# Kernel optimization log

Measured on AMD Instinct MI355X. Metric: run time of the kernel, lower is better.

The kernel has to match this reference:

```python
import jax, jax.numpy as jnp
import numpy as np

EMBED_DIM = 1536
NUM_HEADS = 12
HEAD_DIM = EMBED_DIM // NUM_HEADS  # 128
SEQ = 2048
EPS = 1e-5


def rms_norm(x, w):
    # x: (..., HEAD_DIM)
    var = jnp.mean(jnp.square(x), axis=-1, keepdims=True)
    return x * jax.lax.rsqrt(var + EPS) * w


def apply_rotary(x, cos, sin):
    # x: (b, s, h, d); cos/sin: (s, d/2) -> broadcast (1, s, 1, d/2)
    d2 = cos.shape[-1]
    c = cos[None, :, None, :]
    s_ = sin[None, :, None, :]
    x1, x2 = x[..., :d2], x[..., d2:]
    return jnp.concatenate([x1 * c - x2 * s_, x2 * c + x1 * s_], axis=-1)


def setup_inputs() -> dict:
    key = jax.random.key(0)
    ks = jax.random.split(key, 10)
    x = jax.random.normal(ks[0], (SEQ, 1, EMBED_DIM), dtype=jnp.float32)
    cu_seqlens = jnp.array([0, SEQ // 2, SEQ], dtype=jnp.int32)
    # rotary tables for positions 0..SEQ-1, rotary dim = HEAD_DIM
    inv_freq = 1.0 / (10000.0 ** (jnp.arange(0, HEAD_DIM, 2, dtype=jnp.float32) / HEAD_DIM))
    pos = jnp.arange(SEQ, dtype=jnp.float32)
    freqs = pos[:, None] * inv_freq[None, :]  # (s, d/2)
    rotary_pos_emb_cos = jnp.cos(freqs)
    rotary_pos_emb_sin = jnp.sin(freqs)
    scale = 0.02
    w_qkv = jax.random.normal(ks[1], (EMBED_DIM, 3 * EMBED_DIM), dtype=jnp.float32) * scale
    b_qkv = jnp.zeros((3 * EMBED_DIM,), dtype=jnp.float32)
    q_norm_w = jnp.ones((HEAD_DIM,), dtype=jnp.float32)
    k_norm_w = jnp.ones((HEAD_DIM,), dtype=jnp.float32)
    w_proj = jax.random.normal(ks[2], (EMBED_DIM, EMBED_DIM), dtype=jnp.float32) * scale
    b_proj = jnp.zeros((EMBED_DIM,), dtype=jnp.float32)
    return {
        'x': x, 'cu_seqlens': cu_seqlens,
        'rotary_pos_emb_cos': rotary_pos_emb_cos, 'rotary_pos_emb_sin': rotary_pos_emb_sin,
        'w_qkv': w_qkv, 'b_qkv': b_qkv, 'q_norm_w': q_norm_w, 'k_norm_w': k_norm_w,
        'w_proj': w_proj, 'b_proj': b_proj,
    }


def reference(x, cu_seqlens, rotary_pos_emb_cos, rotary_pos_emb_sin,
              w_qkv, b_qkv, q_norm_w, k_norm_w, w_proj, b_proj):
    s, b, e = x.shape
    h, d = NUM_HEADS, HEAD_DIM
    qkv = jnp.einsum('sbe,ef->sbf', x, w_qkv) + b_qkv  # (s, b, 3e)
    q, k, v = jnp.split(qkv, 3, axis=2)
    q = q.reshape(s, b, h, d)
    k = k.reshape(s, b, h, d)
    v = v.reshape(s, b, h, d)
    # per-head RMSNorm on q/k
    q = rms_norm(q, q_norm_w)
    k = rms_norm(k, k_norm_w)
    # (s, b, h, d) -> (b, s, h, d)
    q = jnp.transpose(q, (1, 0, 2, 3))
    k = jnp.transpose(k, (1, 0, 2, 3))
    v = jnp.transpose(v, (1, 0, 2, 3))
    q = apply_rotary(q, rotary_pos_emb_cos, rotary_pos_emb_sin)
    k = apply_rotary(k, rotary_pos_emb_cos, rotary_pos_emb_sin)
    # varlen (block-diagonal, non-causal) attention via segment mask
    pos = jnp.arange(s)
    seg = jnp.searchsorted(cu_seqlens[1:], pos, side='right')  # (s,)
    mask = seg[:, None] == seg[None, :]  # (s, s)
    scale = d ** -0.5
    scores = jnp.einsum('bqhd,bkhd->bhqk', q, k) * scale  # (b, h, s, s)
    scores = jnp.where(mask[None, None, :, :], scores, jnp.finfo(scores.dtype).min)
    attn = jax.nn.softmax(scores, axis=-1)
    ctx = jnp.einsum('bhqk,bkhd->bqhd', attn, v)  # (b, s, h, d)
    # (b, s, h, d) -> (s, b, h*d)
    ctx = jnp.transpose(ctx, (1, 0, 2, 3)).reshape(s, b, h * d)
    out = jnp.einsum('sbe,ef->sbf', ctx, w_proj) + b_proj
    return out
```

## Files before the change

### kernel.cpp

```cpp
#include <hip/hip_runtime.h>
#include <hip/hip_bf16.h>
#include <stdint.h>

#define S_LEN 2048
#define EMB   1536
#define NH    12
#define HD    128
#define N3    4608
#define RMS_EPS 1e-5f
#define ATTN_SCALE 0.08838834764831845f
#define SPLIT 2
#define LOG2E 1.44269504088896f
#define DEFER_THR 11.5416f

typedef short short8_t __attribute__((ext_vector_type(8)));
typedef float f32x4    __attribute__((ext_vector_type(4)));

typedef __attribute__((address_space(1))) const void g1_void;
typedef __attribute__((address_space(3))) void l3_void;

__device__ __forceinline__ void gload_lds16(const void* g, void* l) {
  __builtin_amdgcn_global_load_lds((g1_void*)g, (l3_void*)l, 16, 0, 0);
}

__device__ __forceinline__ short f2bf(float f) {
  union { float f; unsigned u; } v; v.f = f;
  unsigned r = (v.u + 0x7FFFu + ((v.u >> 16) & 1u)) >> 16;
  return (short)(r & 0xFFFFu);
}
__device__ __forceinline__ float bf2f(short s) {
  union { unsigned u; float f; } v; v.u = ((unsigned)(unsigned short)s) << 16;
  return v.f;
}

__global__ __launch_bounds__(256) void k_cvt_bf16(const float* __restrict__ in,
                                                  short* __restrict__ out, int n) {
  int i = (blockIdx.x * 256 + threadIdx.x) * 4;
  if (i + 3 < n) {
    float4 v = *(const float4*)(in + i);
    short4 o;
    o.x = f2bf(v.x); o.y = f2bf(v.y); o.z = f2bf(v.z); o.w = f2bf(v.w);
    *(short4*)(out + i) = o;
  }
}

__global__ __launch_bounds__(256) void k_transpose_cvt(const float* __restrict__ W,
                                                       short* __restrict__ Wt,
                                                       int K, int N) {
  __shared__ float t[32][33];
  int n0 = blockIdx.x * 32, k0 = blockIdx.y * 32;
  int tx = threadIdx.x, ty = threadIdx.y;
#pragma unroll
  for (int r = 0; r < 4; ++r) {
    int k = ty + r * 8;
    t[k][tx] = W[(size_t)(k0 + k) * N + n0 + tx];
  }
  __syncthreads();
#pragma unroll
  for (int r = 0; r < 4; ++r) {
    int j = ty + r * 8;
    Wt[(size_t)(n0 + j) * K + k0 + tx] = f2bf(t[tx][j]);
  }
}

template<bool OBF>
__global__ __launch_bounds__(256, 2) void k_gemm_v7(const short* __restrict__ A,
                                                    const short* __restrict__ Bt,
                                                    const float* __restrict__ bias,
                                                    void* __restrict__ Cv,
                                                    int M, int N, int K) {
  __shared__ short lds[2][2][128 * 64];
  const int tid = threadIdx.x;
  const int lane = tid & 63, wid = tid >> 6;
  const int wr = (wid >> 1) * 64, wc = (wid & 1) * 64;

  const int nbn = N >> 7;
  const int perbn = nbn >> 2;
  const int x = blockIdx.x & 7;
  const int s = blockIdx.x >> 3;
  const int bm = ((x >> 2) * 8 + (s & 7)) * 128;
  const int bn = ((x & 3) * perbn + (s >> 3)) * 128;

  const int lr = lane & 15, lg = lane >> 4;
  const int swz = (lr & 7) << 4;
  const int srow = lane >> 3;
  const int skc  = ((lane & 7) ^ srow) * 8;

  f32x4 acc[4][4] = {};
  const int nk = K >> 6;

#define GSTAGE(kt_, buf_)                                                          \
  {                                                                                \
    const int kt__ = (kt_);                                                        \
    _Pragma("unroll")                                                              \
    for (int it = 0; it < 4; ++it) {                                               \
      int seg = wid * 4 + it;                                                      \
      int row = seg * 8 + srow;                                                    \
      gload_lds16(A  + (size_t)(bm + row) * K + kt__ + skc, &lds[buf_][0][seg * 512]); \
      gload_lds16(Bt + (size_t)(bn + row) * K + kt__ + skc, &lds[buf_][1][seg * 512]); \
    }                                                                              \
  }

  GSTAGE(0, 0);
  if (nk > 1) {
    GSTAGE(64, 1);
    asm volatile("s_waitcnt vmcnt(8)" ::: "memory");
  } else {
    asm volatile("s_waitcnt vmcnt(0)" ::: "memory");
  }
  __builtin_amdgcn_s_barrier();

  int cur = 0;
  for (int t = 0; t < nk; ++t) {
    const char* baseA = (const char*)&lds[cur][0][0];
    const char* baseB = (const char*)&lds[cur][1][0];

    short8_t af0[4], bf0[4], af1[4], bf1[4];
#pragma unroll
    for (int m = 0; m < 4; ++m) {
      int rowA = wr + m * 16 + lr;
      int rowB = wc + m * 16 + lr;
      af0[m] = *(const short8_t*)(baseA + ((rowA * 128 + 0 * 64 + lg * 16) ^ swz));
      bf0[m] = *(const short8_t*)(baseB + ((rowB * 128 + 0 * 64 + lg * 16) ^ swz));
      af1[m] = *(const short8_t*)(baseA + ((rowA * 128 + 1 * 64 + lg * 16) ^ swz));
      bf1[m] = *(const short8_t*)(baseB + ((rowB * 128 + 1 * 64 + lg * 16) ^ swz));
    }

    __builtin_amdgcn_s_setprio(1);
#pragma unroll
    for (int m = 0; m < 4; ++m)
#pragma unroll
      for (int n = 0; n < 4; ++n)
        acc[m][n] = __builtin_amdgcn_mfma_f32_16x16x32_bf16(af0[m], bf0[n], acc[m][n], 0, 0, 0);
    __builtin_amdgcn_s_setprio(0);

    asm volatile("s_waitcnt lgkmcnt(0)" ::: "memory");
    __builtin_amdgcn_sched_barrier(0);
    __builtin_amdgcn_s_barrier();

    if (t + 2 < nk) GSTAGE((t + 2) << 6, cur);

    __builtin_amdgcn_s_setprio(1);
#pragma unroll
    for (int m = 0; m < 4; ++m)
#pragma unroll
      for (int n = 0; n < 4; ++n)
        acc[m][n] = __builtin_amdgcn_mfma_f32_16x16x32_bf16(af1[m], bf1[n], acc[m][n], 0, 0, 0);
    __builtin_amdgcn_s_setprio(0);

    if (t + 2 < nk) {
      asm volatile("s_waitcnt vmcnt(8)" ::: "memory");
    } else {
      asm volatile("s_waitcnt vmcnt(0)" ::: "memory");
    }
    __builtin_amdgcn_s_barrier();
    cur ^= 1;
  }
#undef GSTAGE

#pragma unroll
  for (int m = 0; m < 4; ++m)
#pragma unroll
    for (int n = 0; n < 4; ++n) {
      int col = bn + wc + n * 16 + lr;
      float bv = bias[col];
#pragma unroll
      for (int r = 0; r < 4; ++r) {
        int row = bm + wr + m * 16 + lg * 4 + r;
        float v = acc[m][n][r] + bv;
        if (OBF) ((short*)Cv)[(size_t)row * N + col] = f2bf(v);
        else     ((float*)Cv)[(size_t)row * N + col] = v;
      }
    }
}

__global__ __launch_bounds__(256) void k_post(const short* __restrict__ qkv,
                                              const float* __restrict__ cosv,
                                              const float* __restrict__ sinv,
                                              const float* __restrict__ qw,
                                              const float* __restrict__ kw,
                                              short* __restrict__ qb,
                                              short* __restrict__ kb,
                                              short* __restrict__ vt) {
  __shared__ short ldsv[64 * 130];
  const int h = blockIdx.x, s0 = blockIdx.y * 64;
  const int t = threadIdx.x;
  const int r = t >> 2, j = t & 3;
  const int s = s0 + r;
  const size_t rowbase = (size_t)s * N3 + h * HD;
  const float SC2 = ATTN_SCALE * LOG2E;

  {
    const short* vp = qkv + rowbase + 2 * EMB + j * 32;
#pragma unroll
    for (int i4 = 0; i4 < 4; ++i4)
      *(short8_t*)&ldsv[r * 130 + j * 32 + i4 * 8] = *(const short8_t*)(vp + i4 * 8);
  }

#pragma unroll
  for (int qk = 0; qk < 2; ++qk) {
    const short* p = qkv + rowbase + qk * EMB + j * 32;
    const float* w = qk ? kw : qw;
    float v[32];
#pragma unroll
    for (int i4 = 0; i4 < 4; ++i4) {
      short8_t x = *(const short8_t*)(p + i4 * 8);
#pragma unroll
      for (int e = 0; e < 8; ++e) v[i4 * 8 + e] = bf2f(x[e]);
    }
    float ss = 0.f;
#pragma unroll
    for (int i = 0; i < 32; ++i) ss += v[i] * v[i];
    ss += __shfl_xor(ss, 1);
    ss += __shfl_xor(ss, 2);
    float rsq = rsqrtf(ss * (1.0f / HD) + RMS_EPS);
    if (qk == 0) rsq *= SC2;
#pragma unroll
    for (int i = 0; i < 32; ++i) v[i] = v[i] * rsq * w[j * 32 + i];
    const float* cp = cosv + (size_t)s * 64 + (j & 1) * 32;
    const float* sp = sinv + (size_t)s * 64 + (j & 1) * 32;
    short out[32];
#pragma unroll
    for (int i = 0; i < 32; ++i) {
      float part = __shfl_xor(v[i], 2);
      float c = cp[i], sn = sp[i];
      float o = (j < 2) ? (v[i] * c - part * sn) : (v[i] * c + part * sn);
      out[i] = f2bf(o);
    }
    short* dst = (qk ? kb : qb) + ((size_t)h * S_LEN + s) * HD + j * 32;
#pragma unroll
    for (int i4 = 0; i4 < 4; ++i4) {
      short8_t o8;
#pragma unroll
      for (int e = 0; e < 8; ++e) o8[e] = out[i4 * 8 + e];
      *(short8_t*)(dst + i4 * 8) = o8;
    }
  }

  __syncthreads();
  const int sl = t & 63, wv = t >> 6;
#pragma unroll
  for (int it = 0; it < 32; ++it) {
    int d = it * 4 + wv;
    vt[((size_t)h * HD + d) * S_LEN + s0 + sl] = ldsv[sl * 130 + d];
  }
}

__global__ __launch_bounds__(512, 2) void k_attn(const short* __restrict__ qb,
                                                 const short* __restrict__ kb,
                                                 const short* __restrict__ vt,
                                                 const int* __restrict__ cu, int nseg,
                                                 short* __restrict__ Opart,
                                                 float* __restrict__ mlpart) {
  __shared__ short ldsK[2][8192];
  __shared__ short ldsV[2][128 * 64];
  __shared__ short ldsP[8 * 16 * 64];

  const int wg = blockIdx.x;
  const int member = wg / 48;
  const int c = wg % 48;
  const int p = c & 1;
  const int h = c >> 2;
  const int qt = ((c >> 1) & 1) * 8 + member;

  const int q0 = qt * 128;
  const int tid = threadIdx.x, l = tid & 63, w = tid >> 6;
  const int lr = l & 15, lg = l >> 4;

  const short* kb_h = kb + (size_t)h * S_LEN * HD;
  const short* vt_h = vt + (size_t)h * HD * S_LEN;

  const int qrow_sm = q0 + w * 16 + lr;
  int segq = 0;
  for (int i = 1; i <= nseg; ++i) if (qrow_sm >= cu[i]) segq = i;
  const int rs_s = (segq == 0) ? 0 : cu[segq];
  const int re_s = (segq < nseg) ? cu[segq + 1] : S_LEN;
  float m = -INFINITY, lsum = 0.f;

  int seg0 = 0, seg1 = 0;
  for (int i = 1; i <= nseg; ++i) {
    if (q0 >= cu[i]) seg0 = i;
    if (q0 + 127 >= cu[i]) seg1 = i;
  }
  const int ks = (seg0 == 0) ? 0 : cu[seg0];
  const int ke = (seg1 < nseg) ? cu[seg1 + 1] : S_LEN;
  const int kt0 = (ks >> 6) << 6;
  const int nt = (ke - kt0 + 63) >> 6;
  const int tpb = (nt + SPLIT - 1) / SPLIT;
  const int tb0 = p * tpb;
  const int tb1 = (tb0 + tpb < nt) ? tb0 + tpb : nt;

  const int vseg_row = l >> 3;

  short8_t qf[4];
  {
    int srow = q0 + w * 16 + lr;
    const short* qp = qb + ((size_t)h * S_LEN + srow) * HD;
#pragma unroll
    for (int kk = 0; kk < 4; ++kk)
      qf[kk] = *(const short8_t*)(qp + kk * 32 + lg * 8);
  }

  f32x4 cacc[8] = {};

#define STAGE(kt_, buf_)                                                          \
  {                                                                               \
    const int kt__ = (kt_);                                                       \
    _Pragma("unroll")                                                             \
    for (int it = 0; it < 2; ++it) {                                              \
      int s = w * 2 + it;                                                         \
      int half = s >> 3;                                                          \
      int krow = (s & 7) * 8 + (l >> 3);                                          \
      int kc = half * 64 + (((l & 7) ^ (l >> 3)) * 8);                            \
      gload_lds16(kb_h + (size_t)(kt__ + krow) * HD + kc, &ldsK[buf_][s * 512]);  \
      int drow = s * 8 + vseg_row;                                                \
      int sv = ((l & 7) ^ (drow & 7)) * 8;                                        \
      gload_lds16(vt_h + (size_t)drow * S_LEN + kt__ + sv, &ldsV[buf_][s * 512]); \
    }                                                                             \
  }

  if (tb0 < tb1)     STAGE(kt0 + tb0 * 64, 0);
  if (tb0 + 1 < tb1) {
    STAGE(kt0 + (tb0 + 1) * 64, 1);
    asm volatile("s_waitcnt vmcnt(4)" ::: "memory");
  } else {
    asm volatile("s_waitcnt vmcnt(0)" ::: "memory");
  }
  __builtin_amdgcn_s_barrier();

  int cur = 0;
  for (int ti = tb0; ti < tb1; ++ti) {
    const int kt = kt0 + ti * 64;
    const char* bK = (const char*)&ldsK[cur][0];
    const char* bV = (const char*)&ldsV[cur][0];

    f32x4 sacc[4] = {};
    __builtin_amdgcn_s_setprio(1);
#pragma unroll
    for (int n = 0; n < 4; ++n) {
#pragma unroll
      for (int kk = 0; kk < 4; ++kk) {
        int row = n * 16 + lr;
        int byte = (kk >> 1) * 8192 + row * 128 + (kk & 1) * 64 + lg * 16;
        byte ^= (lr & 7) << 4;
        short8_t kf = *(const short8_t*)(bK + byte);
        sacc[n] = __builtin_amdgcn_mfma_f32_16x16x32_bf16(kf, qf[kk], sacc[n], 0, 0, 0);
      }
    }
    __builtin_amdgcn_s_setprio(0);

    if (!__all((kt >= rs_s) && (kt + 64 <= re_s))) {
#pragma unroll
      for (int n = 0; n < 4; ++n) {
        int kbase = kt + n * 16 + lg * 4;
#pragma unroll
        for (int r = 0; r < 4; ++r) {
          int key = kbase + r;
          sacc[n][r] = (key >= rs_s && key < re_s) ? sacc[n][r] : -1e30f;
        }
      }
    }

    float tm = sacc[0][0];
#pragma unroll
    for (int n = 0; n < 4; ++n)
#pragma unroll
      for (int r = 0; r < 4; ++r) tm = fmaxf(tm, sacc[n][r]);
    tm = fmaxf(tm, __shfl_xor(tm, 16));
    tm = fmaxf(tm, __shfl_xor(tm, 32));

    if (!__all(tm <= m + DEFER_THR)) {
      float mn = fmaxf(m, tm);
      float alpha = exp2f(m - mn);
      m = mn;
      lsum *= alpha;
      float a[4];
#pragma unroll
      for (int r = 0; r < 4; ++r) a[r] = __shfl(alpha, lg * 4 + r);
#pragma unroll
      for (int n = 0; n < 8; ++n)
#pragma unroll
        for (int r = 0; r < 4; ++r) cacc[n][r] *= a[r];
    }

    float ls = 0.f;
#pragma unroll
    for (int n = 0; n < 4; ++n) {
      short4 p4;
      float p0 = exp2f(sacc[n][0] - m);
      float p1 = exp2f(sacc[n][1] - m);
      float p2 = exp2f(sacc[n][2] - m);
      float p3 = exp2f(sacc[n][3] - m);
      ls += (p0 + p1) + (p2 + p3);
      p4.x = f2bf(p0); p4.y = f2bf(p1); p4.z = f2bf(p2); p4.w = f2bf(p3);
      int byte = lr * 128 + (n * 16 + lg * 4) * 2;
      byte ^= (lr & 7) << 4;
      *(short4*)((char*)ldsP + w * 2048 + byte) = p4;
    }
    ls += __shfl_xor(ls, 16);
    ls += __shfl_xor(ls, 32);
    lsum += ls;

    __builtin_amdgcn_s_setprio(1);
#pragma unroll
    for (int kk = 0; kk < 2; ++kk) {
      int byteP = lr * 128 + (kk * 32 + lg * 8) * 2;
      byteP ^= (lr & 7) << 4;
      short8_t pf = *(const short8_t*)((const char*)ldsP + w * 2048 + byteP);
#pragma unroll
      for (int n = 0; n < 8; ++n) {
        int d = n * 16 + lr;
        int byteV = d * 128 + (kk * 32 + lg * 8) * 2;
        byteV ^= (d & 7) << 4;
        short8_t vf = *(const short8_t*)(bV + byteV);
        cacc[n] = __builtin_amdgcn_mfma_f32_16x16x32_bf16(pf, vf, cacc[n], 0, 0, 0);
      }
    }
    __builtin_amdgcn_s_setprio(0);

    __builtin_amdgcn_s_barrier();
    if (ti + 2 < tb1) {
      STAGE(kt0 + (ti + 2) * 64, cur);
      asm volatile("s_waitcnt vmcnt(4)" ::: "memory");
    } else {
      asm volatile("s_waitcnt vmcnt(0)" ::: "memory");
    }
    __builtin_amdgcn_s_barrier();
    cur ^= 1;
  }
#undef STAGE

  const int b = (h * 16 + qt) * SPLIT + p;
#pragma unroll
  for (int r = 0; r < 4; ++r) {
    int qrow = w * 16 + lg * 4 + r;
#pragma unroll
    for (int n = 0; n < 8; ++n)
      Opart[(size_t)b * 16384 + qrow * 128 + n * 16 + lr] = f2bf(cacc[n][r]);
  }
  if (lg == 0) {
    mlpart[(size_t)b * 256 + w * 16 + lr] = m;
    mlpart[(size_t)b * 256 + 128 + w * 16 + lr] = lsum;
  }
}

__global__ __launch_bounds__(512) void k_combine(const short* __restrict__ Opart,
                                                 const float* __restrict__ ml,
                                                 short* __restrict__ ctx) {
  const int h = blockIdx.x, qt = blockIdx.y, t = threadIdx.x;
  const int r = t >> 2, j = t & 3;
  const int b0 = (h * 16 + qt) * SPLIT;

  float mp[SPLIT], lp[SPLIT], wp[SPLIT];
  float M = -INFINITY;
#pragma unroll
  for (int p = 0; p < SPLIT; ++p) {
    mp[p] = ml[(size_t)(b0 + p) * 256 + r];
    lp[p] = ml[(size_t)(b0 + p) * 256 + 128 + r];
    M = fmaxf(M, mp[p]);
  }
  float L = 0.f;
#pragma unroll
  for (int p = 0; p < SPLIT; ++p) {
    wp[p] = exp2f(mp[p] - M);
    L += lp[p] * wp[p];
  }
  const float inv = 1.0f / L;

  float acc[32];
#pragma unroll
  for (int i = 0; i < 32; ++i) acc[i] = 0.f;
#pragma unroll
  for (int p = 0; p < SPLIT; ++p) {
    const short* src = Opart + (size_t)(b0 + p) * 16384 + r * 128 + j * 32;
#pragma unroll
    for (int i4 = 0; i4 < 4; ++i4) {
      short8_t v = *(const short8_t*)(src + i4 * 8);
#pragma unroll
      for (int e = 0; e < 8; ++e) acc[i4 * 8 + e] += wp[p] * bf2f(v[e]);
    }
  }

  short* dst = ctx + (size_t)(qt * 128 + r) * EMB + h * HD + j * 32;
#pragma unroll
  for (int i4 = 0; i4 < 4; ++i4) {
    short8_t o8;
#pragma unroll
    for (int e = 0; e < 8; ++e) o8[e] = f2bf(acc[i4 * 8 + e] * inv);
    *(short8_t*)(dst + i4 * 8) = o8;
  }
}

extern "C" void kernel_launch(void* const* d_in, const int* in_sizes, int n_in,
                              void* d_out, int out_size, void* d_ws, size_t ws_size,
                              hipStream_t stream) {
  const float* x      = (const float*)d_in[0];
  const int*   cu     = (const int*)d_in[1];
  const float* cosv   = (const float*)d_in[2];
  const float* sinv   = (const float*)d_in[3];
  const float* w_qkv  = (const float*)d_in[4];
  const float* b_qkv  = (const float*)d_in[5];
  const float* q_norm = (const float*)d_in[6];
  const float* k_norm = (const float*)d_in[7];
  const float* w_proj = (const float*)d_in[8];
  const float* b_proj = (const float*)d_in[9];
  const int nseg = in_sizes[1] - 1;

  char* ws = (char*)d_ws;
  short* xb     = (short*)(ws);
  short* wqkvT  = (short*)(ws + 6291456);
  short* wprojT = (short*)(ws + 20447232);
  short* qkv16  = (short*)(ws + 25165824);
  short* qb     = (short*)(ws + 44040192);
  short* kb     = (short*)(ws + 50331648);
  short* vt     = (short*)(ws + 56623104);
  short* ctxb   = (short*)(ws + 62914560);
  short* Opart  = qkv16;
  float* mlpart = (float*)ws;

  k_cvt_bf16<<<(S_LEN * EMB) / 1024, 256, 0, stream>>>(x, xb, S_LEN * EMB);
  k_transpose_cvt<<<dim3(N3 / 32, EMB / 32), dim3(32, 8), 0, stream>>>(w_qkv, wqkvT, EMB, N3);
  k_transpose_cvt<<<dim3(EMB / 32, EMB / 32), dim3(32, 8), 0, stream>>>(w_proj, wprojT, EMB, EMB);
  k_gemm_v7<true><<<dim3((N3 / 128) * (S_LEN / 128)), 256, 0, stream>>>(xb, wqkvT, b_qkv, qkv16, S_LEN, N3, EMB);
  k_post<<<dim3(NH, S_LEN / 64), 256, 0, stream>>>(qkv16, cosv, sinv, q_norm, k_norm, qb, kb, vt);
  k_attn<<<dim3(NH * (S_LEN / 128) * SPLIT), 512, 0, stream>>>(qb, kb, vt, cu, nseg, Opart, mlpart);
  k_combine<<<dim3(NH, S_LEN / 128), 512, 0, stream>>>(Opart, mlpart, ctxb);
  k_gemm_v7<false><<<dim3((EMB / 128) * (S_LEN / 128)), 256, 0, stream>>>(ctxb, wprojT, b_proj, (float*)d_out, S_LEN, EMB, EMB);
}
```

Measured before the change: 130.7 us.

## Split-K the QKV GEMM into two halves and sum partials in post kernel

Replaces the QKV projection GEMM with a split-K version that launches twice as many blocks (two K halves), each writing a bf16 partial result to a separate buffer. The post-processing kernel then reads both partials and adds them before RMSNorm, rotary and the V transpose. The new GEMM drops the double-buffered LDS pipeline in favour of a single buffer with higher occupancy. The aim is better CU utilisation for the 576-tile GEMM. The cost is extra memory traffic for the second partial buffer, and the separate bf16 rounding of each partial lowers precision.

```diff
diff --git a/kernel.cpp b/kernel.cpp
--- a/kernel.cpp
+++ b/kernel.cpp
@@ -63,6 +63,78 @@
   }
 }
 
+__global__ __launch_bounds__(256, 4) void k_gemm_v8(const short* __restrict__ A,
+                                                    const short* __restrict__ Bt,
+                                                    const float* __restrict__ bias,
+                                                    short* __restrict__ C0,
+                                                    short* __restrict__ C1,
+                                                    int M, int N, int K) {
+  __shared__ short lds[2][128 * 64];
+  const int tid = threadIdx.x;
+  const int lane = tid & 63, wid = tid >> 6;
+  const int wr = (wid >> 1) * 64, wc = (wid & 1) * 64;
+  const int bn = blockIdx.x * 128, bm = blockIdx.y * 128;
+  const int z = blockIdx.z;
+  const int lr = lane & 15, lg = lane >> 4;
+  const int swz = (lr & 7) << 4;
+
+  const int srow = lane >> 3;
+  const int skc  = ((lane & 7) ^ srow) * 8;
+
+  f32x4 acc[4][4] = {};
+  const int kh = K >> 1;
+  const int k0 = z * kh;
+  const int nk = kh >> 6;
+
+  for (int t = 0; t < nk; ++t) {
+    const int kt = k0 + (t << 6);
+    __syncthreads();
+#pragma unroll
+    for (int it = 0; it < 4; ++it) {
+      int seg = wid * 4 + it;
+      int row = seg * 8 + srow;
+      gload_lds16(A  + (size_t)(bm + row) * K + kt + skc, &lds[0][seg * 512]);
+      gload_lds16(Bt + (size_t)(bn + row) * K + kt + skc, &lds[1][seg * 512]);
+    }
+    __syncthreads();
+    const char* baseA = (const char*)&lds[0][0];
+    const char* baseB = (const char*)&lds[1][0];
+#pragma unroll
+    for (int kk = 0; kk < 2; ++kk) {
+      short8_t af[4], bfr[4];
+#pragma unroll
+      for (int m = 0; m < 4; ++m) {
+        int row = wr + m * 16 + lr;
+        af[m] = *(const short8_t*)(baseA + ((row * 128 + kk * 64 + lg * 16) ^ swz));
+      }
+#pragma unroll
+      for (int n = 0; n < 4; ++n) {
+        int row = wc + n * 16 + lr;
+        bfr[n] = *(const short8_t*)(baseB + ((row * 128 + kk * 64 + lg * 16) ^ swz));
+      }
+#pragma unroll
+      for (int m = 0; m < 4; ++m)
+#pragma unroll
+        for (int n = 0; n < 4; ++n)
+          acc[m][n] = __builtin_amdgcn_mfma_f32_16x16x32_bf16(af[m], bfr[n], acc[m][n], 0, 0, 0);
+    }
+  }
+
+  short* C = z ? C1 : C0;
+#pragma unroll
+  for (int m = 0; m < 4; ++m)
+#pragma unroll
+    for (int n = 0; n < 4; ++n) {
+      int col = bn + wc + n * 16 + lr;
+      float bv = z ? 0.f : bias[col];
+#pragma unroll
+      for (int r = 0; r < 4; ++r) {
+        int row = bm + wr + m * 16 + lg * 4 + r;
+        C[(size_t)row * N + col] = f2bf(acc[m][n][r] + bv);
+      }
+    }
+}
+
 template<bool OBF>
 __global__ __launch_bounds__(256, 2) void k_gemm_v7(const short* __restrict__ A,
                                                     const short* __restrict__ Bt,
@@ -174,13 +246,14 @@
     }
 }
 
-__global__ __launch_bounds__(256) void k_post(const short* __restrict__ qkv,
+__global__ __launch_bounds__(256) void k_post(const short* __restrict__ qkvA,
+                                              const short* __restrict__ qkvB,
                                               const float* __restrict__ cosv,
                                               const float* __restrict__ sinv,
                                               const float* __restrict__ qw,
                                               const float* __restrict__ kw,
-                                              short* __restrict__ qb,
-                                              short* __restrict__ kb,
+                                              short* __restrict__ qbo,
+                                              short* __restrict__ kbo,
                                               short* __restrict__ vt) {
   __shared__ short ldsv[64 * 130];
   const int h = blockIdx.x, s0 = blockIdx.y * 64;
@@ -191,22 +264,31 @@
   const float SC2 = ATTN_SCALE * LOG2E;
 
   {
-    const short* vp = qkv + rowbase + 2 * EMB + j * 32;
-#pragma unroll
-    for (int i4 = 0; i4 < 4; ++i4)
-      *(short8_t*)&ldsv[r * 130 + j * 32 + i4 * 8] = *(const short8_t*)(vp + i4 * 8);
+    const short* va = qkvA + rowbase + 2 * EMB + j * 32;
+    const short* vb = qkvB + rowbase + 2 * EMB + j * 32;
+#pragma unroll
+    for (int i4 = 0; i4 < 4; ++i4) {
+      short8_t xa = *(const short8_t*)(va + i4 * 8);
+      short8_t xb = *(const short8_t*)(vb + i4 * 8);
+      short8_t o8;
+#pragma unroll
+      for (int e = 0; e < 8; ++e) o8[e] = f2bf(bf2f(xa[e]) + bf2f(xb[e]));
+      *(short8_t*)&ldsv[r * 130 + j * 32 + i4 * 8] = o8;
+    }
   }
 
 #pragma unroll
   for (int qk = 0; qk < 2; ++qk) {
-    const short* p = qkv + rowbase + qk * EMB + j * 32;
+    const short* pa = qkvA + rowbase + qk * EMB + j * 32;
+    const short* pb = qkvB + rowbase + qk * EMB + j * 32;
     const float* w = qk ? kw : qw;
     float v[32];
 #pragma unroll
     for (int i4 = 0; i4 < 4; ++i4) {
-      short8_t x = *(const short8_t*)(p + i4 * 8);
-#pragma unroll
-      for (int e = 0; e < 8; ++e) v[i4 * 8 + e] = bf2f(x[e]);
+      short8_t xa = *(const short8_t*)(pa + i4 * 8);
+      short8_t xb = *(const short8_t*)(pb + i4 * 8);
+#pragma unroll
+      for (int e = 0; e < 8; ++e) v[i4 * 8 + e] = bf2f(xa[e]) + bf2f(xb[e]);
     }
     float ss = 0.f;
 #pragma unroll
@@ -227,7 +309,7 @@
       float o = (j < 2) ? (v[i] * c - part * sn) : (v[i] * c + part * sn);
       out[i] = f2bf(o);
     }
-    short* dst = (qk ? kb : qb) + ((size_t)h * S_LEN + s) * HD + j * 32;
+    short* dst = (qk ? kbo : qbo) + ((size_t)h * S_LEN + s) * HD + j * 32;
 #pragma unroll
     for (int i4 = 0; i4 < 4; ++i4) {
       short8_t o8;
@@ -510,19 +592,20 @@
   short* xb     = (short*)(ws);
   short* wqkvT  = (short*)(ws + 6291456);
   short* wprojT = (short*)(ws + 20447232);
-  short* qkv16  = (short*)(ws + 25165824);
+  short* qkvA   = (short*)(ws + 25165824);
   short* qb     = (short*)(ws + 44040192);
   short* kb     = (short*)(ws + 50331648);
   short* vt     = (short*)(ws + 56623104);
   short* ctxb   = (short*)(ws + 62914560);
-  short* Opart  = qkv16;
+  short* qkvB   = (short*)(ws + 69206016);
+  short* Opart  = qkvA;
   float* mlpart = (float*)ws;
 
   k_cvt_bf16<<<(S_LEN * EMB) / 1024, 256, 0, stream>>>(x, xb, S_LEN * EMB);
   k_transpose_cvt<<<dim3(N3 / 32, EMB / 32), dim3(32, 8), 0, stream>>>(w_qkv, wqkvT, EMB, N3);
   k_transpose_cvt<<<dim3(EMB / 32, EMB / 32), dim3(32, 8), 0, stream>>>(w_proj, wprojT, EMB, EMB);
-  k_gemm_v7<true><<<dim3((N3 / 128) * (S_LEN / 128)), 256, 0, stream>>>(xb, wqkvT, b_qkv, qkv16, S_LEN, N3, EMB);
-  k_post<<<dim3(NH, S_LEN / 64), 256, 0, stream>>>(qkv16, cosv, sinv, q_norm, k_norm, qb, kb, vt);
+  k_gemm_v8<<<dim3(N3 / 128, S_LEN / 128, 2), 256, 0, stream>>>(xb, wqkvT, b_qkv, qkvA, qkvB, S_LEN, N3, EMB);
+  k_post<<<dim3(NH, S_LEN / 64), 256, 0, stream>>>(qkvA, qkvB, cosv, sinv, q_norm, k_norm, qb, kb, vt);
   k_attn<<<dim3(NH * (S_LEN / 128) * SPLIT), 512, 0, stream>>>(qb, kb, vt, cu, nseg, Opart, mlpart);
   k_combine<<<dim3(NH, S_LEN / 128), 512, 0, stream>>>(Opart, mlpart, ctxb);
   k_gemm_v7<false><<<dim3((EMB / 128) * (S_LEN / 128)), 256, 0, stream>>>(ctxb, wprojT, b_proj, (float*)d_out, S_LEN, EMB, EMB);
```

After: 136.4 us. +4.4%, slower.

## Fuse prep conversions into one launch and split attention KV across three parts

Applied to the files above, without the earlier changes.

Merges the x bf16 conversion and both weight transpose-convert kernels into a single k_prep launch, which dispatches on block index, to cut launch overhead. Raises the attention KV split from 2 to 3 and remaps the workgroup index so that 576 workgroups run instead of 384, to fill more compute units on the MI355X. The extra split means more partial outputs and more combine work. Whether combine and the Opart/mlpart buffers handle SPLIT=3 correctly depends on code that is not shown.

```diff
diff --git a/kernel.cpp b/kernel.cpp
--- a/kernel.cpp
+++ b/kernel.cpp
@@ -9,7 +9,7 @@
 #define N3    4608
 #define RMS_EPS 1e-5f
 #define ATTN_SCALE 0.08838834764831845f
-#define SPLIT 2
+#define SPLIT 3
 #define LOG2E 1.44269504088896f
 #define DEFER_THR 11.5416f
 
@@ -33,23 +33,33 @@
   return v.f;
 }
 
-__global__ __launch_bounds__(256) void k_cvt_bf16(const float* __restrict__ in,
-                                                  short* __restrict__ out, int n) {
-  int i = (blockIdx.x * 256 + threadIdx.x) * 4;
-  if (i + 3 < n) {
-    float4 v = *(const float4*)(in + i);
+__global__ __launch_bounds__(256) void k_prep(const float* __restrict__ x,
+                                              const float* __restrict__ w_qkv,
+                                              const float* __restrict__ w_proj,
+                                              short* __restrict__ xb,
+                                              short* __restrict__ wqkvT,
+                                              short* __restrict__ wprojT) {
+  const int z = blockIdx.x, tid = threadIdx.x;
+  if (z < 3072) {
+    int i = z * 1024 + tid * 4;
+    float4 v = *(const float4*)(x + i);
     short4 o;
     o.x = f2bf(v.x); o.y = f2bf(v.y); o.z = f2bf(v.z); o.w = f2bf(v.w);
-    *(short4*)(out + i) = o;
-  }
-}
-
-__global__ __launch_bounds__(256) void k_transpose_cvt(const float* __restrict__ W,
-                                                       short* __restrict__ Wt,
-                                                       int K, int N) {
+    *(short4*)(xb + i) = o;
+    return;
+  }
   __shared__ float t[32][33];
-  int n0 = blockIdx.x * 32, k0 = blockIdx.y * 32;
-  int tx = threadIdx.x, ty = threadIdx.y;
+  const float* W; short* Wt; int K, N, n0, k0;
+  if (z < 9984) {
+    int idx = z - 3072;
+    W = w_qkv; Wt = wqkvT; K = EMB; N = N3;
+    n0 = (idx % 144) * 32; k0 = (idx / 144) * 32;
+  } else {
+    int idx = z - 9984;
+    W = w_proj; Wt = wprojT; K = EMB; N = EMB;
+    n0 = (idx % 48) * 32; k0 = (idx / 48) * 32;
+  }
+  const int tx = tid & 31, ty = tid >> 5;
 #pragma unroll
   for (int r = 0; r < 4; ++r) {
     int k = ty + r * 8;
@@ -179,8 +189,8 @@
                                               const float* __restrict__ sinv,
                                               const float* __restrict__ qw,
                                               const float* __restrict__ kw,
-                                              short* __restrict__ qb,
-                                              short* __restrict__ kb,
+                                              short* __restrict__ qbo,
+                                              short* __restrict__ kbo,
                                               short* __restrict__ vt) {
   __shared__ short ldsv[64 * 130];
   const int h = blockIdx.x, s0 = blockIdx.y * 64;
@@ -204,9 +214,9 @@
     float v[32];
 #pragma unroll
     for (int i4 = 0; i4 < 4; ++i4) {
-      short8_t x = *(const short8_t*)(p + i4 * 8);
-#pragma unroll
-      for (int e = 0; e < 8; ++e) v[i4 * 8 + e] = bf2f(x[e]);
+      short8_t xv = *(const short8_t*)(p + i4 * 8);
+#pragma unroll
+      for (int e = 0; e < 8; ++e) v[i4 * 8 + e] = bf2f(xv[e]);
     }
     float ss = 0.f;
 #pragma unroll
@@ -227,7 +237,7 @@
       float o = (j < 2) ? (v[i] * c - part * sn) : (v[i] * c + part * sn);
       out[i] = f2bf(o);
     }
-    short* dst = (qk ? kb : qb) + ((size_t)h * S_LEN + s) * HD + j * 32;
+    short* dst = (qk ? kbo : qbo) + ((size_t)h * S_LEN + s) * HD + j * 32;
 #pragma unroll
     for (int i4 = 0; i4 < 4; ++i4) {
       short8_t o8;
@@ -257,11 +267,12 @@
   __shared__ short ldsP[8 * 16 * 64];
 
   const int wg = blockIdx.x;
-  const int member = wg / 48;
-  const int c = wg % 48;
-  const int p = c & 1;
-  const int h = c >> 2;
-  const int qt = ((c >> 1) & 1) * 8 + member;
+  const int member = wg / 72;
+  const int c = wg % 72;
+  const int p = c % 3;
+  const int hs = c / 3;
+  const int h = hs >> 1;
+  const int qt = (hs & 1) * 8 + member;
 
   const int q0 = qt * 128;
   const int tid = threadIdx.x, l = tid & 63, w = tid >> 6;
@@ -518,12 +529,10 @@
   short* Opart  = qkv16;
   float* mlpart = (float*)ws;
 
-  k_cvt_bf16<<<(S_LEN * EMB) / 1024, 256, 0, stream>>>(x, xb, S_LEN * EMB);
-  k_transpose_cvt<<<dim3(N3 / 32, EMB / 32), dim3(32, 8), 0, stream>>>(w_qkv, wqkvT, EMB, N3);
-  k_transpose_cvt<<<dim3(EMB / 32, EMB / 32), dim3(32, 8), 0, stream>>>(w_proj, wprojT, EMB, EMB);
+  k_prep<<<12288, 256, 0, stream>>>(x, w_qkv, w_proj, xb, wqkvT, wprojT);
   k_gemm_v7<true><<<dim3((N3 / 128) * (S_LEN / 128)), 256, 0, stream>>>(xb, wqkvT, b_qkv, qkv16, S_LEN, N3, EMB);
   k_post<<<dim3(NH, S_LEN / 64), 256, 0, stream>>>(qkv16, cosv, sinv, q_norm, k_norm, qb, kb, vt);
-  k_attn<<<dim3(NH * (S_LEN / 128) * SPLIT), 512, 0, stream>>>(qb, kb, vt, cu, nseg, Opart, mlpart);
+  k_attn<<<dim3(NH * 16 * SPLIT), 512, 0, stream>>>(qb, kb, vt, cu, nseg, Opart, mlpart);
   k_combine<<<dim3(NH, S_LEN / 128), 512, 0, stream>>>(Opart, mlpart, ctxb);
   k_gemm_v7<false><<<dim3((EMB / 128) * (S_LEN / 128)), 256, 0, stream>>>(ctxb, wprojT, b_proj, (float*)d_out, S_LEN, EMB, EMB);
 }
```

Result: faster. 128.0 us, median of 3 (-2.0%).
